# Performance work log

Measured on AMD Instinct MI355X. Metric: run time of the kernel, lower is better.

Reference implementation:

```python
import jax, jax.numpy as jnp
import numpy as np

B, T, DIM = 2, 2048, 2048
H, HKV, HD = 16, 4, 128
ROPE_BASE = 10000.0
RMS_EPS = 1.1920929e-07  # torch F.rms_norm default eps = finfo(fp32).eps


def setup_inputs() -> dict:
    key = jax.random.key(0)
    ks = jax.random.split(key, 5)
    s = DIM ** -0.5
    return {
        "x": jax.random.normal(ks[0], (B, T, DIM), jnp.float32),
        "Wq": jax.random.normal(ks[1], (DIM, DIM), jnp.float32) * s,
        "Wk": jax.random.normal(ks[2], (DIM, HKV * HD), jnp.float32) * s,
        "Wv": jax.random.normal(ks[3], (DIM, HKV * HD), jnp.float32) * s,
        "Wo": jax.random.normal(ks[4], (DIM, DIM), jnp.float32) * s,
        "q_gain": jnp.ones((H,), jnp.float32),
    }


def _rms_norm(x):
    return x * jax.lax.rsqrt(jnp.mean(x * x, axis=-1, keepdims=True) + RMS_EPS)


def _rotary(t, hd, base, dtype):
    inv_freq = base ** (-jnp.arange(0, hd, 2, dtype=jnp.float32) / hd)  # [hd/2]
    ang = jnp.arange(t, dtype=jnp.float32)[:, None] * inv_freq[None, :]  # [T, hd/2]
    return jnp.cos(ang).astype(dtype), jnp.sin(ang).astype(dtype)


def _apply_rope(x, cos, sin):
    # x: [B, h, T, D]; cos/sin: [T, D/2] broadcast over batch/heads
    d = x.shape[-1] // 2
    x1, x2 = x[..., :d], x[..., d:]
    return jnp.concatenate([x1 * cos + x2 * sin, -x1 * sin + x2 * cos], axis=-1)


def reference(x, Wq, Wk, Wv, Wo, q_gain):
    Bq, Tq, _ = x.shape
    q = (x @ Wq).reshape(Bq, Tq, H, HD).transpose(0, 2, 1, 3)      # [B,H,T,D]
    k = (x @ Wk).reshape(Bq, Tq, HKV, HD).transpose(0, 2, 1, 3)    # [B,Hkv,T,D]
    v = (x @ Wv).reshape(Bq, Tq, HKV, HD).transpose(0, 2, 1, 3)    # [B,Hkv,T,D]
    q = _rms_norm(q)
    k = _rms_norm(k)
    cos, sin = _rotary(Tq, HD, ROPE_BASE, q.dtype)
    q = _apply_rope(q, cos, sin)
    k = _apply_rope(k, cos, sin)
    q = q * q_gain.astype(q.dtype)[None, :, None, None]
    g = H // HKV
    qg = q.reshape(Bq, HKV, g, Tq, HD)
    # causal GQA SDPA
    scores = jnp.einsum('bkgqd,bkld->bkgql', qg, k) * (HD ** -0.5)
    causal = jnp.tril(jnp.ones((Tq, Tq), bool))
    scores = jnp.where(causal, scores, -jnp.inf)
    p = jax.nn.softmax(scores, axis=-1)
    yg = jnp.einsum('bkgql,bkld->bkgqd', p, v)                      # [B,Hkv,g,T,D]
    # XSA: remove component of each output along the token's own value vector
    vn = v / jnp.clip(jnp.linalg.norm(v, axis=-1, keepdims=True), 1e-12)
    vn = vn[:, :, None]                                             # [B,Hkv,1,T,D]
    proj = jnp.sum(yg * vn, axis=-1, keepdims=True) * vn
    y = (yg - proj).reshape(Bq, H, Tq, HD)
    y = y.transpose(0, 2, 1, 3).reshape(Bq, Tq, DIM)
    return y @ Wo
```

## Files before the change

### kernel.cpp

```cpp
#include <hip/hip_runtime.h>

constexpr int SL  = 2048;
constexpr int NB  = 2;
constexpr int NH  = 16;
constexpr int NKV = 4;
constexpr int HDIM = 128;
constexpr int DM  = 2048;

typedef unsigned short u16;
typedef unsigned int   u32;
typedef short s16x8 __attribute__((ext_vector_type(8)));
typedef float f32x4 __attribute__((ext_vector_type(4)));

__device__ inline u16 f2bf(float x) {
  union { float f; u32 u; } c; c.f = x;
  u32 r = c.u + 0x7fffu + ((c.u >> 16) & 1u);
  return (u16)(r >> 16);
}
__device__ inline float bf2f(u16 h) {
  union { u32 u; float f; } c; c.u = ((u32)h) << 16; return c.f;
}
__device__ inline u32 cvtpk_bf16(float lo, float hi) {
  u32 r;
  asm("v_cvt_pk_bf16_f32 %0, %1, %2" : "=v"(r) : "v"(lo), "v"(hi));
  return r;
}

__device__ inline void gload16(const void* g, void* l) {
  __builtin_amdgcn_global_load_lds((const __attribute__((address_space(1))) void*)g,
                                   (__attribute__((address_space(3))) void*)l, 16, 0, 0);
}

__global__ __launch_bounds__(256) void prep(const float* __restrict__ x,
                                            const float* __restrict__ Wq,
                                            const float* __restrict__ Wk,
                                            const float* __restrict__ Wv,
                                            const float* __restrict__ Wo,
                                            u16* __restrict__ xb,
                                            u16* __restrict__ WT,
                                            u16* __restrict__ WoT) {
  __shared__ float ld[64][65];
  int id = blockIdx.x;
  if (id < 4096) {
    long i = ((long)id * 256 + threadIdx.x) * 8;
    float4 a = *(const float4*)(x + i);
    float4 b = *(const float4*)(x + i + 4);
    uint4 ov;
    ov.x = (u32)f2bf(a.x) | ((u32)f2bf(a.y) << 16);
    ov.y = (u32)f2bf(a.z) | ((u32)f2bf(a.w) << 16);
    ov.z = (u32)f2bf(b.x) | ((u32)f2bf(b.y) << 16);
    ov.w = (u32)f2bf(b.z) | ((u32)f2bf(b.w) << 16);
    *(uint4*)(xb + i) = ov;
    return;
  }
  id -= 4096;
  const float* src; u16* dst; int N; long bx, by;
  const int K = 2048;
  if (id < 1024)      { src = Wq; dst = WT;                         N = 2048; bx = id & 31; by = id >> 5; }
  else if (id < 1280) { int j = id - 1024; src = Wk; dst = WT + (size_t)2048 * 2048; N = 512; bx = j & 7; by = j >> 3; }
  else if (id < 1536) { int j = id - 1280; src = Wv; dst = WT + (size_t)2560 * 2048; N = 512; bx = j & 7; by = j >> 3; }
  else                { int j = id - 1536; src = Wo; dst = WoT;                     N = 2048; bx = j & 31; by = j >> 5; }
  int tid = threadIdx.x;
  long c0 = bx * 64, r0 = by * 64;
  for (int i = 0; i < 16; ++i) {
    int e = tid + 256 * i;
    int r = e >> 6, c = e & 63;
    ld[r][c] = src[(r0 + r) * N + c0 + c];
  }
  __syncthreads();
  for (int i = 0; i < 16; ++i) {
    int e = tid + 256 * i;
    int r = e >> 6, c = e & 63;
    dst[(c0 + r) * K + r0 + c] = f2bf(ld[c][r]);
  }
}

template <int BF16OUT>
__global__ __launch_bounds__(256) void gemm_bt(const u16* __restrict__ A,
                                               const u16* __restrict__ BT,
                                               float* __restrict__ Cf,
                                               u16* __restrict__ Cb,
                                               int M, int N, int K) {
  __shared__ __align__(16) char As[2][128 * 128];
  __shared__ __align__(16) char Bs[2][128 * 128];
  const int tid = threadIdx.x;
  const int lane = tid & 63;
  const int w = tid >> 6;
  const int wm = w >> 1, wn = w & 1;
  const int lr = lane & 15, lg = lane >> 4;
  const long bm = (long)blockIdx.x * 128;
  const long bn = (long)blockIdx.y * 128;

  f32x4 acc[4][4] = {};

  auto stage = [&](int kt0, int buf) {
#pragma unroll
    for (int i = 0; i < 4; ++i) {
      int c = tid + 256 * i;
      int row = c >> 3;
      int slot = (c & 7) << 4;
      int gs = slot ^ ((row & 7) << 4);
      gload16(A + (bm + row) * K + kt0 + (gs >> 1), As[buf] + c * 16);
    }
#pragma unroll
    for (int i = 0; i < 4; ++i) {
      int c = tid + 256 * i;
      int row = c >> 3;
      int slot = (c & 7) << 4;
      int gs = slot ^ ((row & 7) << 4);
      gload16(BT + (bn + row) * K + kt0 + (gs >> 1), Bs[buf] + c * 16);
    }
  };

  const int nt = K >> 6;
  stage(0, 0);

#pragma unroll 1
  for (int ti = 0; ti < nt; ++ti) {
    const int cur = ti & 1;
    if (ti + 1 < nt) {
      stage((ti + 1) << 6, cur ^ 1);
      asm volatile("s_waitcnt vmcnt(8)" ::: "memory");
    } else {
      asm volatile("s_waitcnt vmcnt(0)" ::: "memory");
    }
    __builtin_amdgcn_s_barrier();

    __builtin_amdgcn_s_setprio(1);
#pragma unroll
    for (int kk = 0; kk < 2; ++kk) {
      int colB = (kk * 32 + lg * 8) * 2;
      s16x8 af[4], bfv[4];
#pragma unroll
      for (int m = 0; m < 4; ++m) {
        int row = wm * 64 + m * 16 + lr;
        af[m] = *(const s16x8*)(As[cur] + row * 128 + (colB ^ ((row & 7) << 4)));
      }
#pragma unroll
      for (int n = 0; n < 4; ++n) {
        int row = wn * 64 + n * 16 + lr;
        bfv[n] = *(const s16x8*)(Bs[cur] + row * 128 + (colB ^ ((row & 7) << 4)));
      }
#pragma unroll
      for (int m = 0; m < 4; ++m)
#pragma unroll
        for (int n = 0; n < 4; ++n)
          acc[m][n] = __builtin_amdgcn_mfma_f32_16x16x32_bf16(af[m], bfv[n], acc[m][n], 0, 0, 0);
    }
    __builtin_amdgcn_s_setprio(0);
    __builtin_amdgcn_s_barrier();
  }

#pragma unroll
  for (int m = 0; m < 4; ++m)
#pragma unroll
    for (int n = 0; n < 4; ++n) {
      long row = bm + wm * 64 + m * 16 + lg * 4;
      long col = bn + wn * 64 + n * 16 + lr;
#pragma unroll
      for (int r = 0; r < 4; ++r) {
        if (BF16OUT)
          Cb[(row + r) * N + col] = f2bf(acc[m][n][r]);
        else
          Cf[(row + r) * N + col] = acc[m][n][r];
      }
    }
}

__global__ __launch_bounds__(256) void postqkv(const u16* __restrict__ qkv,
                                               const float* __restrict__ qg,
                                               u16* __restrict__ qb, u16* __restrict__ kb,
                                               u16* __restrict__ vt) {
  __shared__ u16 ldt[64][136];
  int id = blockIdx.x;
  int tid = threadIdx.x;
  if (id < 4096) {
    int token = id;
    int b = token >> 11, t = token & (SL - 1);
    int lane = tid & 63, w = tid >> 6;
    const u16* row = qkv + (long)token * 3072;
    float inv = __expf(-(float)lane * (9.210340371976184f / 64.0f));
    float ang = (float)t * inv;
    float c = cosf(ang), s = sinf(ang);
    for (int slot = w; slot < 20; slot += 4) {
      const u16* p = row + slot * 128;
      float v0 = bf2f(p[lane]), v1 = bf2f(p[lane + 64]);
      float ss = v0 * v0 + v1 * v1;
      for (int m = 1; m < 64; m <<= 1) ss += __shfl_xor(ss, m);
      float rms = rsqrtf(ss * (1.0f / 128.0f) + 1.1920929e-07f);
      v0 *= rms; v1 *= rms;
      float o0 =  v0 * c + v1 * s;
      float o1 = -v0 * s + v1 * c;
      u16* dst;
      if (slot < 16) {
        float g = qg[slot] * 0.08838834764831845f * 1.4426950408889634f;
        o0 *= g; o1 *= g;
        dst = qb + ((long)(b * NH + slot) * SL + t) * 128;
      } else {
        dst = kb + ((long)(b * NKV + (slot - 16)) * SL + t) * 128;
      }
      dst[lane] = f2bf(o0);
      dst[lane + 64] = f2bf(o1);
    }
    return;
  }
  int blk = id - 4096;
  int tt = blk & 31, kvb = blk >> 5;
  const u16* src = qkv + (long)(((kvb >> 2) * SL) + tt * 64) * 3072 + 2560 + (kvb & 3) * 128;
  for (int i = 0; i < 32; ++i) {
    int e = tid + 256 * i;
    int r = e >> 7, d = e & 127;
    ldt[r][d] = src[(long)r * 3072 + d];
  }
  __syncthreads();
  u16* dst = vt + (long)kvb * 128 * SL + tt * 64;
  for (int i = 0; i < 32; ++i) {
    int o = tid + 256 * i;
    int d = o >> 6, r = o & 63;
    dst[(long)d * SL + r] = ldt[r][d];
  }
}

__global__ __launch_bounds__(256) void attn(const u16* __restrict__ qb, const u16* __restrict__ kb,
                                            const u16* __restrict__ vt, u16* __restrict__ yg) {
  __shared__ __align__(16) char Ks[2][64 * 256];
  __shared__ __align__(16) char Vs[2][128 * 128];
  __shared__ __align__(16) char Ps[64 * 128];
  const int tid = threadIdx.x, lane = tid & 63, w = tid >> 6;
  const int pairIdx = blockIdx.x;
  const int bh = blockIdx.y;
  const int b = bh >> 4, h = bh & 15;
  const int kvh = h >> 2;
  const int lr = lane & 15, lg = lane >> 4;

  const u16* kbase = kb + (long)(b * NKV + kvh) * SL * 128;
  const u16* vbase = vt + (long)(b * NKV + kvh) * 128 * SL;

#pragma unroll 1
  for (int pass = 0; pass < 2; ++pass) {
    const int qblk = pass ? 31 - pairIdx : pairIdx;
    const int ntile = qblk + 1;

    const u16* qp = qb + ((long)bh * SL + qblk * 64 + w * 16 + lr) * 128;
    s16x8 qf[4];
#pragma unroll
    for (int kk = 0; kk < 4; ++kk) qf[kk] = *(const s16x8*)(qp + kk * 32 + lg * 8);

    f32x4 acc[8] = {};
    float m_run[4], l_run[4];
#pragma unroll
    for (int r = 0; r < 4; ++r) { m_run[r] = -1e30f; l_run[r] = 0.f; }

#pragma unroll
    for (int i = 0; i < 4; ++i) {
      int c = tid + 256 * i;
      int row = c >> 4, slot = (c & 15) << 4;
      gload16(kbase + (long)row * 128 + ((slot ^ ((row & 15) << 4)) >> 1), Ks[0] + c * 16);
    }
#pragma unroll
    for (int i = 0; i < 4; ++i) {
      int c = tid + 256 * i;
      int row = c >> 3, slot = (c & 7) << 4;
      gload16(vbase + (long)row * SL + ((slot ^ ((row & 7) << 4)) >> 1), Vs[0] + c * 16);
    }

#pragma unroll 1
    for (int kt = 0; kt < ntile; ++kt) {
      const int cur = kt & 1;
      if (kt + 1 < ntile) {
        const int nx = cur ^ 1;
#pragma unroll
        for (int i = 0; i < 4; ++i) {
          int c = tid + 256 * i;
          int row = c >> 4, slot = (c & 15) << 4;
          gload16(kbase + (long)((kt + 1) * 64 + row) * 128 + ((slot ^ ((row & 15) << 4)) >> 1),
                  Ks[nx] + c * 16);
        }
#pragma unroll
        for (int i = 0; i < 4; ++i) {
          int c = tid + 256 * i;
          int row = c >> 3, slot = (c & 7) << 4;
          gload16(vbase + (long)row * SL + (kt + 1) * 64 + ((slot ^ ((row & 7) << 4)) >> 1),
                  Vs[nx] + c * 16);
        }
        asm volatile("s_waitcnt vmcnt(8)" ::: "memory");
      } else {
        asm volatile("s_waitcnt vmcnt(0)" ::: "memory");
      }
      __builtin_amdgcn_s_barrier();

      f32x4 sv[4];
      __builtin_amdgcn_s_setprio(1);
#pragma unroll
      for (int n = 0; n < 4; ++n) {
        f32x4 z = {0.f, 0.f, 0.f, 0.f};
#pragma unroll
        for (int kk = 0; kk < 4; ++kk) {
          int row = n * 16 + lr;
          s16x8 kf = *(const s16x8*)(Ks[cur] + row * 256 + (((kk * 32 + lg * 8) * 2) ^ ((row & 15) << 4)));
          z = __builtin_amdgcn_mfma_f32_16x16x32_bf16(qf[kk], kf, z, 0, 0, 0);
        }
        sv[n] = z;
      }
      __builtin_amdgcn_s_setprio(0);

      if (kt == qblk) {
#pragma unroll
        for (int n = 0; n < 4; ++n)
#pragma unroll
          for (int r = 0; r < 4; ++r) {
            int colA = n * 16 + lr;
            int rowA = w * 16 + lg * 4 + r;
            if (colA > rowA) sv[n][r] = -1e30f;
          }
      }
      float mx[4];
#pragma unroll
      for (int r = 0; r < 4; ++r)
        mx[r] = fmaxf(fmaxf(sv[0][r], sv[1][r]), fmaxf(sv[2][r], sv[3][r]));
#pragma unroll
      for (int r = 0; r < 4; ++r) {
        float v = mx[r];
        v = fmaxf(v, __shfl_xor(v, 1));
        v = fmaxf(v, __shfl_xor(v, 2));
        v = fmaxf(v, __shfl_xor(v, 4));
        v = fmaxf(v, __shfl_xor(v, 8));
        mx[r] = v;
      }
      bool okb = true;
#pragma unroll
      for (int r = 0; r < 4; ++r) okb = okb && (mx[r] <= m_run[r] + 8.0f);
      if (!__all(okb ? 1 : 0)) {
        float alpha[4];
#pragma unroll
        for (int r = 0; r < 4; ++r) {
          float mn = fmaxf(m_run[r], mx[r]);
          alpha[r] = __builtin_amdgcn_exp2f(m_run[r] - mn);
          m_run[r] = mn;
          l_run[r] *= alpha[r];
        }
#pragma unroll
        for (int n = 0; n < 8; ++n) {
          f32x4 a = acc[n];
#pragma unroll
          for (int r = 0; r < 4; ++r) a[r] *= alpha[r];
          acc[n] = a;
        }
      }
      float rsum[4] = {0.f, 0.f, 0.f, 0.f};
#pragma unroll
      for (int n = 0; n < 4; ++n)
#pragma unroll
        for (int r = 0; r < 4; ++r) {
          float p = __builtin_amdgcn_exp2f(sv[n][r] - m_run[r]);
          sv[n][r] = p;
          rsum[r] += p;
        }
#pragma unroll
      for (int r = 0; r < 4; ++r) {
        float v = rsum[r];
        v += __shfl_xor(v, 1);
        v += __shfl_xor(v, 2);
        v += __shfl_xor(v, 4);
        v += __shfl_xor(v, 8);
        l_run[r] += v;
      }
#pragma unroll
      for (int n = 0; n < 4; ++n) {
        u32 pk0 = cvtpk_bf16(sv[n][0], sv[n][1]);
        u32 pk1 = cvtpk_bf16(sv[n][2], sv[n][3]);
        int row = w * 16 + lg * 4;
        int colB = (n * 16 + lr) * 2;
        *(u16*)(Ps + (row + 0) * 128 + (colB ^ (((row + 0) & 7) << 4))) = (u16)pk0;
        *(u16*)(Ps + (row + 1) * 128 + (colB ^ (((row + 1) & 7) << 4))) = (u16)(pk0 >> 16);
        *(u16*)(Ps + (row + 2) * 128 + (colB ^ (((row + 2) & 7) << 4))) = (u16)pk1;
        *(u16*)(Ps + (row + 3) * 128 + (colB ^ (((row + 3) & 7) << 4))) = (u16)(pk1 >> 16);
      }
      __builtin_amdgcn_s_setprio(1);
#pragma unroll
      for (int kk = 0; kk < 2; ++kk) {
        int prow = w * 16 + lr;
        s16x8 pa = *(const s16x8*)(Ps + prow * 128 + (((kk * 32 + lg * 8) * 2) ^ ((prow & 7) << 4)));
#pragma unroll
        for (int n = 0; n < 8; ++n) {
          int vrow = n * 16 + lr;
          s16x8 vf = *(const s16x8*)(Vs[cur] + vrow * 128 + (((kk * 32 + lg * 8) * 2) ^ ((vrow & 7) << 4)));
          acc[n] = __builtin_amdgcn_mfma_f32_16x16x32_bf16(pa, vf, acc[n], 0, 0, 0);
        }
      }
      __builtin_amdgcn_s_setprio(0);
      __builtin_amdgcn_s_barrier();
    }

    float inv_l[4];
#pragma unroll
    for (int r = 0; r < 4; ++r) inv_l[r] = 1.0f / l_run[r];
    u16* yp = yg + ((long)bh * SL + qblk * 64 + w * 16 + lg * 4) * 128;
#pragma unroll
    for (int n = 0; n < 8; ++n)
#pragma unroll
      for (int r = 0; r < 4; ++r)
        yp[(long)r * 128 + n * 16 + lr] = f2bf(acc[n][r] * inv_l[r]);
  }
}

__global__ __launch_bounds__(256) void epi(const u16* __restrict__ yg,
                                           const u16* __restrict__ qkv,
                                           u16* __restrict__ yb) {
  __shared__ float vn[4][128];
  int token = blockIdx.x;
  int b = token >> 11, t = token & (SL - 1);
  int lane = threadIdx.x & 63, w = threadIdx.x >> 6;
  const u16* vp = qkv + (long)token * 3072 + 2560 + w * 128;
  float v0 = bf2f(vp[lane]), v1 = bf2f(vp[lane + 64]);
  float ss = v0 * v0 + v1 * v1;
  for (int m = 1; m < 64; m <<= 1) ss += __shfl_xor(ss, m);
  float inv = 1.0f / fmaxf(sqrtf(ss), 1e-12f);
  vn[w][lane] = v0 * inv;
  vn[w][lane + 64] = v1 * inv;
  __syncthreads();
  for (int hi = 0; hi < 4; ++hi) {
    int h = w * 4 + hi;
    const u16* yp = yg + ((long)(b * NH + h) * SL + t) * 128;
    float y0 = bf2f(yp[lane]), y1 = bf2f(yp[lane + 64]);
    float n0 = vn[w][lane], n1 = vn[w][lane + 64];
    float d = y0 * n0 + y1 * n1;
    for (int m = 1; m < 64; m <<= 1) d += __shfl_xor(d, m);
    y0 -= d * n0;
    y1 -= d * n1;
    u16* dst = yb + (long)token * DM + h * 128;
    dst[lane] = f2bf(y0);
    dst[lane + 64] = f2bf(y1);
  }
}

extern "C" void kernel_launch(void* const* d_in, const int* in_sizes, int n_in,
                              void* d_out, int out_size, void* d_ws, size_t ws_size,
                              hipStream_t stream) {
  const float* x  = (const float*)d_in[0];
  const float* Wq = (const float*)d_in[1];
  const float* Wk = (const float*)d_in[2];
  const float* Wv = (const float*)d_in[3];
  const float* Wo = (const float*)d_in[4];
  const float* qg = (const float*)d_in[5];
  float* out = (float*)d_out;

  char* p = (char*)d_ws;
  u16* xb    = (u16*)p;   p += (size_t)4096 * 2048 * 2;
  u16* WT    = (u16*)p;   p += (size_t)3072 * 2048 * 2;
  u16* WoT   = (u16*)p;   p += (size_t)2048 * 2048 * 2;
  u16* qkvb  = (u16*)p;   p += (size_t)4096 * 3072 * 2;
  u16* qbuf  = (u16*)p;   p += (size_t)NB * NH * SL * 128 * 2;
  u16* kbuf  = (u16*)p;   p += (size_t)NB * NKV * SL * 128 * 2;
  u16* vtb   = (u16*)p;   p += (size_t)NB * NKV * 128 * SL * 2;
  u16* ygb   = (u16*)p;   p += (size_t)NB * NH * SL * 128 * 2;
  u16* yb = xb;

  prep<<<6656, 256, 0, stream>>>(x, Wq, Wk, Wv, Wo, xb, WT, WoT);
  gemm_bt<1><<<dim3(32, 24), 256, 0, stream>>>(xb, WT, nullptr, qkvb, 4096, 3072, 2048);
  postqkv<<<4352, 256, 0, stream>>>(qkvb, qg, qbuf, kbuf, vtb);
  attn<<<dim3(16, 32), 256, 0, stream>>>(qbuf, kbuf, vtb, ygb);
  epi<<<4096, 256, 0, stream>>>(ygb, qkvb, yb);
  gemm_bt<0><<<dim3(32, 16), 256, 0, stream>>>(yb, WoT, out, nullptr, 4096, 2048, 2048);
}
```

Baseline: 242.8 us.

## Use static softmax bound from RMS-norm in attention and vectorize transposes

```diff
diff --git a/kernel.cpp b/kernel.cpp
--- a/kernel.cpp
+++ b/kernel.cpp
@@ -62,16 +62,27 @@
   else                { int j = id - 1536; src = Wo; dst = WoT;                     N = 2048; bx = j & 31; by = j >> 5; }
   int tid = threadIdx.x;
   long c0 = bx * 64, r0 = by * 64;
-  for (int i = 0; i < 16; ++i) {
+#pragma unroll
+  for (int i = 0; i < 4; ++i) {
     int e = tid + 256 * i;
-    int r = e >> 6, c = e & 63;
-    ld[r][c] = src[(r0 + r) * N + c0 + c];
+    int r = e >> 4, cg = e & 15;
+    float4 v = *(const float4*)(src + (r0 + r) * N + c0 + cg * 4);
+    ld[r][cg * 4 + 0] = v.x;
+    ld[r][cg * 4 + 1] = v.y;
+    ld[r][cg * 4 + 2] = v.z;
+    ld[r][cg * 4 + 3] = v.w;
   }
   __syncthreads();
-  for (int i = 0; i < 16; ++i) {
+#pragma unroll
+  for (int i = 0; i < 4; ++i) {
     int e = tid + 256 * i;
-    int r = e >> 6, c = e & 63;
-    dst[(c0 + r) * K + r0 + c] = f2bf(ld[c][r]);
+    int cg = e & 15, rr = e >> 4;
+    ushort4 o;
+    o.x = f2bf(ld[cg * 4 + 0][rr]);
+    o.y = f2bf(ld[cg * 4 + 1][rr]);
+    o.z = f2bf(ld[cg * 4 + 2][rr]);
+    o.w = f2bf(ld[cg * 4 + 3][rr]);
+    *(ushort4*)(dst + (c0 + rr) * K + r0 + cg * 4) = o;
   }
 }
 
@@ -207,22 +218,31 @@
   int blk = id - 4096;
   int tt = blk & 31, kvb = blk >> 5;
   const u16* src = qkv + (long)(((kvb >> 2) * SL) + tt * 64) * 3072 + 2560 + (kvb & 3) * 128;
-  for (int i = 0; i < 32; ++i) {
+#pragma unroll
+  for (int i = 0; i < 4; ++i) {
     int e = tid + 256 * i;
-    int r = e >> 7, d = e & 127;
-    ldt[r][d] = src[(long)r * 3072 + d];
+    int r = e >> 4, dg = e & 15;
+    uint4 v = *(const uint4*)(src + (long)r * 3072 + dg * 8);
+    *(uint4*)(&ldt[r][dg * 8]) = v;
   }
   __syncthreads();
   u16* dst = vt + (long)kvb * 128 * SL + tt * 64;
-  for (int i = 0; i < 32; ++i) {
-    int o = tid + 256 * i;
-    int d = o >> 6, r = o & 63;
-    dst[(long)d * SL + r] = ldt[r][d];
+#pragma unroll
+  for (int i = 0; i < 8; ++i) {
+    int e = tid + 256 * i;
+    int rg = e & 15, d = e >> 4;
+    ushort4 o;
+    o.x = ldt[rg * 4 + 0][d];
+    o.y = ldt[rg * 4 + 1][d];
+    o.z = ldt[rg * 4 + 2][d];
+    o.w = ldt[rg * 4 + 3][d];
+    *(ushort4*)(dst + (long)d * SL + rg * 4) = o;
   }
 }
 
 __global__ __launch_bounds__(256) void attn(const u16* __restrict__ qb, const u16* __restrict__ kb,
-                                            const u16* __restrict__ vt, u16* __restrict__ yg) {
+                                            const u16* __restrict__ vt, const float* __restrict__ qg,
+                                            u16* __restrict__ yg) {
   __shared__ __align__(16) char Ks[2][64 * 256];
   __shared__ __align__(16) char Vs[2][128 * 128];
   __shared__ __align__(16) char Ps[64 * 128];
@@ -233,6 +253,8 @@
   const int kvh = h >> 2;
   const int lr = lane & 15, lg = lane >> 4;
 
+  const float Ms = 16.3223f * fabsf(qg[h]);
+
   const u16* kbase = kb + (long)(b * NKV + kvh) * SL * 128;
   const u16* vbase = vt + (long)(b * NKV + kvh) * 128 * SL;
 
@@ -247,9 +269,7 @@
     for (int kk = 0; kk < 4; ++kk) qf[kk] = *(const s16x8*)(qp + kk * 32 + lg * 8);
 
     f32x4 acc[8] = {};
-    float m_run[4], l_run[4];
-#pragma unroll
-    for (int r = 0; r < 4; ++r) { m_run[r] = -1e30f; l_run[r] = 0.f; }
+    float lsum[4] = {0.f, 0.f, 0.f, 0.f};
 
 #pragma unroll
     for (int i = 0; i < 4; ++i) {
@@ -314,57 +334,14 @@
             if (colA > rowA) sv[n][r] = -1e30f;
           }
       }
-      float mx[4];
-#pragma unroll
-      for (int r = 0; r < 4; ++r)
-        mx[r] = fmaxf(fmaxf(sv[0][r], sv[1][r]), fmaxf(sv[2][r], sv[3][r]));
-#pragma unroll
-      for (int r = 0; r < 4; ++r) {
-        float v = mx[r];
-        v = fmaxf(v, __shfl_xor(v, 1));
-        v = fmaxf(v, __shfl_xor(v, 2));
-        v = fmaxf(v, __shfl_xor(v, 4));
-        v = fmaxf(v, __shfl_xor(v, 8));
-        mx[r] = v;
-      }
-      bool okb = true;
-#pragma unroll
-      for (int r = 0; r < 4; ++r) okb = okb && (mx[r] <= m_run[r] + 8.0f);
-      if (!__all(okb ? 1 : 0)) {
-        float alpha[4];
+#pragma unroll
+      for (int n = 0; n < 4; ++n)
 #pragma unroll
         for (int r = 0; r < 4; ++r) {
-          float mn = fmaxf(m_run[r], mx[r]);
-          alpha[r] = __builtin_amdgcn_exp2f(m_run[r] - mn);
-          m_run[r] = mn;
-          l_run[r] *= alpha[r];
+          float p = __builtin_amdgcn_exp2f(sv[n][r] - Ms);
+          sv[n][r] = p;
+          lsum[r] += p;
         }
-#pragma unroll
-        for (int n = 0; n < 8; ++n) {
-          f32x4 a = acc[n];
-#pragma unroll
-          for (int r = 0; r < 4; ++r) a[r] *= alpha[r];
-          acc[n] = a;
-        }
-      }
-      float rsum[4] = {0.f, 0.f, 0.f, 0.f};
-#pragma unroll
-      for (int n = 0; n < 4; ++n)
-#pragma unroll
-        for (int r = 0; r < 4; ++r) {
-          float p = __builtin_amdgcn_exp2f(sv[n][r] - m_run[r]);
-          sv[n][r] = p;
-          rsum[r] += p;
-        }
-#pragma unroll
-      for (int r = 0; r < 4; ++r) {
-        float v = rsum[r];
-        v += __shfl_xor(v, 1);
-        v += __shfl_xor(v, 2);
-        v += __shfl_xor(v, 4);
-        v += __shfl_xor(v, 8);
-        l_run[r] += v;
-      }
 #pragma unroll
       for (int n = 0; n < 4; ++n) {
         u32 pk0 = cvtpk_bf16(sv[n][0], sv[n][1]);
@@ -394,7 +371,14 @@
 
     float inv_l[4];
 #pragma unroll
-    for (int r = 0; r < 4; ++r) inv_l[r] = 1.0f / l_run[r];
+    for (int r = 0; r < 4; ++r) {
+      float v = lsum[r];
+      v += __shfl_xor(v, 1);
+      v += __shfl_xor(v, 2);
+      v += __shfl_xor(v, 4);
+      v += __shfl_xor(v, 8);
+      inv_l[r] = 1.0f / v;
+    }
     u16* yp = yg + ((long)bh * SL + qblk * 64 + w * 16 + lg * 4) * 128;
 #pragma unroll
     for (int n = 0; n < 8; ++n)
@@ -459,7 +443,7 @@
   prep<<<6656, 256, 0, stream>>>(x, Wq, Wk, Wv, Wo, xb, WT, WoT);
   gemm_bt<1><<<dim3(32, 24), 256, 0, stream>>>(xb, WT, nullptr, qkvb, 4096, 3072, 2048);
   postqkv<<<4352, 256, 0, stream>>>(qkvb, qg, qbuf, kbuf, vtb);
-  attn<<<dim3(16, 32), 256, 0, stream>>>(qbuf, kbuf, vtb, ygb);
+  attn<<<dim3(16, 32), 256, 0, stream>>>(qbuf, kbuf, vtb, qg, ygb);
   epi<<<4096, 256, 0, stream>>>(ygb, qkvb, yb);
   gemm_bt<0><<<dim3(32, 16), 256, 0, stream>>>(yb, WoT, out, nullptr, 4096, 2048, 2048);
 }
```

After: 213.8 us. 12.0% less time.
